# Kernel tuning notes

Hardware: AMD Instinct MI355X
Metric: run time of the kernel (lower is better)

The kernel has to match this reference:

```python
import jax, jax.numpy as jnp
import numpy as np

HEADS = 8
IN_CH = 768
INNER = 768
DK = INNER // HEADS


def setup_inputs() -> dict:
    key = jax.random.key(0)
    ks = jax.random.split(key, 9)
    bs, hw = 16, 1024
    s = 1.0 / np.sqrt(IN_CH)
    sp = 1.0 / np.sqrt(INNER)
    return {
        "x": jax.random.normal(ks[0], (bs, hw, IN_CH), jnp.float32),
        # weights stored (in, out) so y = x @ W + b (equiv to torch Linear)
        "Wq": jax.random.uniform(ks[1], (IN_CH, INNER), jnp.float32, -s, s),
        "bq": jax.random.uniform(ks[2], (INNER,), jnp.float32, -s, s),
        "Wk": jax.random.uniform(ks[3], (IN_CH, INNER), jnp.float32, -s, s),
        "bk": jax.random.uniform(ks[4], (INNER,), jnp.float32, -s, s),
        "Wv": jax.random.uniform(ks[5], (IN_CH, INNER), jnp.float32, -s, s),
        "bv": jax.random.uniform(ks[6], (INNER,), jnp.float32, -s, s),
        "Wp": jax.random.uniform(ks[7], (INNER, IN_CH), jnp.float32, -sp, sp),
        "bp": jax.random.uniform(ks[8], (IN_CH,), jnp.float32, -sp, sp),
    }


def reference(x, Wq, bq, Wk, bk, Wv, bv, Wp, bp):
    bs, hw, _ = x.shape
    # NOTE: the original torch code does .view(bs, heads, hw, dk) on a
    # (bs, hw, inner) tensor — a raw row-major reshape, not a head-split
    # transpose. Replicate exactly.
    q = (x @ Wq + bq).reshape(bs, HEADS, hw, DK)
    k = (x @ Wk + bk).reshape(bs, HEADS, hw, DK)
    v = (x @ Wv + bv).reshape(bs, HEADS, hw, DK)
    logits = jnp.einsum("bhqd,bhkd->bhqk", q, k) / np.sqrt(DK).astype(np.float32)
    attn = jax.nn.softmax(logits, axis=-1)
    out = jnp.einsum("bhqk,bhkd->bhqd", attn, v).reshape(bs, hw, INNER)
    # dropout is identity in eval mode
    return out @ Wp + bp
```

## Files before the change

### kernel.cpp

```cpp
#include <hip/hip_runtime.h>
#include <math.h>

typedef __bf16 bf16;
typedef __attribute__((ext_vector_type(8))) __bf16 bf16x8;
typedef __attribute__((ext_vector_type(4))) __bf16 bf16x4;
typedef __attribute__((ext_vector_type(4))) float f32x4;
typedef __attribute__((ext_vector_type(16))) float f32x16;

#define CE 0.14724445f

__global__ __launch_bounds__(256) void cvt_x(const float* __restrict__ x, bf16* __restrict__ xb) {
    size_t i = ((size_t)blockIdx.x * 256 + threadIdx.x) * 4;
    f32x4 v = *(const f32x4*)(x + i);
    bf16x4 o;
    o[0] = (bf16)v[0]; o[1] = (bf16)v[1]; o[2] = (bf16)v[2]; o[3] = (bf16)v[3];
    *(bf16x4*)(xb + i) = o;
}

struct WArgs { const float* w[4]; };

__global__ __launch_bounds__(256) void transpose_w(WArgs wa, bf16* __restrict__ out) {
    __shared__ float t[32][33];
    const int z = blockIdx.z;
    const float* __restrict__ W = wa.w[z];
    bf16* __restrict__ Wt = out + (size_t)z * 589824;
    int k0 = blockIdx.x * 32, n0 = blockIdx.y * 32;
    int tx = threadIdx.x, ty = threadIdx.y;
#pragma unroll
    for (int j = 0; j < 4; ++j)
        t[ty + j * 8][tx] = W[(size_t)(k0 + ty + j * 8) * 768 + n0 + tx];
    __syncthreads();
#pragma unroll
    for (int j = 0; j < 4; ++j)
        Wt[(size_t)(n0 + ty + j * 8) * 768 + k0 + tx] = (bf16)t[tx][ty + j * 8];
}

struct GemmArgs {
    const bf16* Bt[3];
    const float* bias[3];
    void* out[3];
};

template <bool F32OUT>
__global__ __launch_bounds__(256, 2) void gemm_kernel(const bf16* __restrict__ A, GemmArgs ga) {
    __shared__ __align__(16) bf16 As[128 * 64];
    __shared__ __align__(16) bf16 Bs[128 * 64];
    const int z = blockIdx.z;
    const bf16* __restrict__ Bt = ga.Bt[z];
    const int m0 = blockIdx.x * 128;
    const int n0 = blockIdx.y * 128;
    const int tid = threadIdx.x;
    const int lane = tid & 63, l15 = lane & 15, lq = lane >> 4;
    const int wid = tid >> 6;
    const int wm = (wid >> 1) * 64, wn = (wid & 1) * 64;

    f32x4 acc[4][4] = {};

    const int srow = tid >> 1;
    const int sc0 = (tid & 1) * 4;
    const bf16* __restrict__ Arow = A + (size_t)(m0 + srow) * 768;
    const bf16* __restrict__ Brow = Bt + (size_t)(n0 + srow) * 768;
    const int swz = srow & 7;

    for (int ks = 0; ks < 768; ks += 64) {
#pragma unroll
        for (int i = 0; i < 4; ++i) {
            int c = sc0 + i;
            bf16x8 av = *(const bf16x8*)(Arow + ks + c * 8);
            bf16x8 bv = *(const bf16x8*)(Brow + ks + c * 8);
            int sc = c ^ swz;
            *(bf16x8*)(As + srow * 64 + sc * 8) = av;
            *(bf16x8*)(Bs + srow * 64 + sc * 8) = bv;
        }
        __syncthreads();
#pragma unroll
        for (int kk = 0; kk < 2; ++kk) {
            bf16x8 af[4], bfr[4];
#pragma unroll
            for (int f = 0; f < 4; ++f) {
                int ar = wm + f * 16 + l15;
                int ac = (kk * 4 + lq) ^ (ar & 7);
                af[f] = *(const bf16x8*)(As + ar * 64 + ac * 8);
                int br = wn + f * 16 + l15;
                int bc = (kk * 4 + lq) ^ (br & 7);
                bfr[f] = *(const bf16x8*)(Bs + br * 64 + bc * 8);
            }
#pragma unroll
            for (int mf = 0; mf < 4; ++mf)
#pragma unroll
                for (int nf = 0; nf < 4; ++nf)
                    acc[mf][nf] = __builtin_amdgcn_mfma_f32_16x16x32_bf16(af[mf], bfr[nf], acc[mf][nf], 0, 0, 0);
        }
        __syncthreads();
    }
    const float* __restrict__ bias = ga.bias[z];
#pragma unroll
    for (int nf = 0; nf < 4; ++nf) {
        int col = n0 + wn + nf * 16 + l15;
        float bv = bias[col];
#pragma unroll
        for (int mf = 0; mf < 4; ++mf) {
            int rbase = m0 + wm + mf * 16 + lq * 4;
#pragma unroll
            for (int i = 0; i < 4; ++i) {
                float v = acc[mf][nf][i] + bv;
                if constexpr (F32OUT)
                    ((float*)ga.out[z])[(size_t)(rbase + i) * 768 + col] = v;
                else
                    ((bf16*)ga.out[z])[(size_t)(rbase + i) * 768 + col] = (bf16)v;
            }
        }
    }
}

__global__ __launch_bounds__(256) void transpose_v(const bf16* __restrict__ V, bf16* __restrict__ Vt) {
    __shared__ unsigned short t[64 * 97];
    const int g = blockIdx.y;
    const int kv0 = blockIdx.x * 64;
    const unsigned short* __restrict__ Vg = (const unsigned short*)V + (size_t)g * 98304;
    unsigned short* __restrict__ Vtg = (unsigned short*)Vt + (size_t)g * 98304;
    const int tid = threadIdx.x;
#pragma unroll
    for (int p = 0; p < 24; ++p) {
        int id = tid + p * 256;
        int row = id / 96, col = id % 96;
        t[row * 97 + col] = Vg[(size_t)(kv0 + row) * 96 + col];
    }
    __syncthreads();
#pragma unroll
    for (int p = 0; p < 24; ++p) {
        int id = tid + p * 256;
        int d = id >> 6, j = id & 63;
        Vtg[(size_t)d * 1024 + kv0 + j] = t[j * 97 + d];
    }
}

static __device__ inline int pk2(float a, float b) {
    union { __bf16 h[2]; int w; } u;
    u.h[0] = (__bf16)a; u.h[1] = (__bf16)b;
    return u.w;
}

static __device__ inline bf16x8 pack_step(float p0, float p1, float p2, float p3,
                                          float p4, float p5, float p6, float p7, int hi) {
    int A0 = pk2(p0, p1), A1 = pk2(p2, p3);
    int B0 = pk2(p4, p5), B1 = pk2(p6, p7);
    int t0 = hi ? A0 : B0;
    int t1 = hi ? A1 : B1;
    int x0 = __shfl_xor(t0, 32);
    int x1 = __shfl_xor(t1, 32);
    union { int w[4]; bf16x8 v; } u;
    u.w[0] = hi ? x0 : A0;
    u.w[1] = hi ? x1 : A1;
    u.w[2] = hi ? B0 : x0;
    u.w[3] = hi ? B1 : x1;
    return u.v;
}

__global__ __launch_bounds__(256, 3) void attn_kernel(const bf16* __restrict__ Q, const bf16* __restrict__ K,
                                                      const bf16* __restrict__ Vt, bf16* __restrict__ AO) {
    __shared__ __align__(16) bf16 Ks[64 * 128];
    __shared__ __align__(16) bf16 Vs[96 * 64];
    const int g = blockIdx.x;
    const int q0 = blockIdx.y * 128;
    const int tid = threadIdx.x;
    const int lane = tid & 63;
    const int l31 = lane & 31;
    const int hi = lane >> 5;
    const int wid = tid >> 6;
    const int qrow = q0 + wid * 32 + l31;
    const int sw = l31 & 7;
    const size_t gbase = (size_t)g * 98304;
    const bf16* __restrict__ Qg = Q + gbase;
    const bf16* __restrict__ Kg = K + gbase;
    const bf16* __restrict__ Vg = Vt + gbase;
    bf16* __restrict__ Og = AO + gbase;

    int koff[3], kld[3], voff[3], vld[3];
#pragma unroll
    for (int i = 0; i < 3; ++i) {
        int id = tid + i * 256;
        int kr = id / 12, kc = id - kr * 12;
        koff[i] = kr * 96 + kc * 8;
        kld[i] = kr * 128 + (kc ^ (kr & 7)) * 8;
        int vr = id >> 3, vc = id & 7;
        voff[i] = vr * 1024 + vc * 8;
        vld[i] = vr * 64 + (vc ^ (vr & 7)) * 8;
    }

    bf16x8 qf[6];
#pragma unroll
    for (int kk = 0; kk < 6; ++kk)
        qf[kk] = *(const bf16x8*)(Qg + (size_t)qrow * 96 + kk * 16 + hi * 8);

    f32x16 o[3] = {};
    float mrun = -INFINITY, lrun = 0.f;

    bf16x8 kst[3], vst[3];
#pragma unroll
    for (int i = 0; i < 3; ++i) {
        kst[i] = *(const bf16x8*)(Kg + koff[i]);
        vst[i] = *(const bf16x8*)(Vg + voff[i]);
    }

    for (int kt = 0; kt < 16; ++kt) {
        __syncthreads();
#pragma unroll
        for (int i = 0; i < 3; ++i) {
            *(bf16x8*)(Ks + kld[i]) = kst[i];
            *(bf16x8*)(Vs + vld[i]) = vst[i];
        }
        __syncthreads();
        if (kt < 15) {
            const int kvn = (kt + 1) * 64;
#pragma unroll
            for (int i = 0; i < 3; ++i) {
                kst[i] = *(const bf16x8*)(Kg + (size_t)kvn * 96 + koff[i]);
                vst[i] = *(const bf16x8*)(Vg + kvn + voff[i]);
            }
        }

        f32x16 s0 = {}, s1 = {};
#pragma unroll
        for (int kk = 0; kk < 6; ++kk) {
            int slot = ((kk * 2 + hi) ^ sw) * 8;
            bf16x8 k0 = *(const bf16x8*)(Ks + l31 * 128 + slot);
            bf16x8 k1 = *(const bf16x8*)(Ks + (l31 + 32) * 128 + slot);
            s0 = __builtin_amdgcn_mfma_f32_32x32x16_bf16(k0, qf[kk], s0, 0, 0, 0);
            s1 = __builtin_amdgcn_mfma_f32_32x32x16_bf16(k1, qf[kk], s1, 0, 0, 0);
        }
        float mx = s0[0];
#pragma unroll
        for (int r = 1; r < 16; ++r) mx = fmaxf(mx, s0[r]);
#pragma unroll
        for (int r = 0; r < 16; ++r) mx = fmaxf(mx, s1[r]);
        mx = fmaxf(mx, __shfl_xor(mx, 32));
        float newm = fmaxf(mrun, mx);
        float alpha = __builtin_amdgcn_exp2f(CE * (mrun - newm));
        mrun = newm;
        float lsum = 0.f;
#pragma unroll
        for (int r = 0; r < 16; ++r) {
            float p = __builtin_amdgcn_exp2f(CE * (s0[r] - newm));
            s0[r] = p; lsum += p;
        }
#pragma unroll
        for (int r = 0; r < 16; ++r) {
            float p = __builtin_amdgcn_exp2f(CE * (s1[r] - newm));
            s1[r] = p; lsum += p;
        }
        lsum += __shfl_xor(lsum, 32);
        lrun = lrun * alpha + lsum;
#pragma unroll
        for (int df = 0; df < 3; ++df)
#pragma unroll
            for (int r = 0; r < 16; ++r) o[df][r] *= alpha;

        bf16x8 pb0 = pack_step(s0[0], s0[1], s0[2], s0[3], s0[4], s0[5], s0[6], s0[7], hi);
        bf16x8 pb1 = pack_step(s0[8], s0[9], s0[10], s0[11], s0[12], s0[13], s0[14], s0[15], hi);
        bf16x8 pb2 = pack_step(s1[0], s1[1], s1[2], s1[3], s1[4], s1[5], s1[6], s1[7], hi);
        bf16x8 pb3 = pack_step(s1[8], s1[9], s1[10], s1[11], s1[12], s1[13], s1[14], s1[15], hi);
#pragma unroll
        for (int df = 0; df < 3; ++df) {
            const bf16* vrow = Vs + (df * 32 + l31) * 64;
            bf16x8 v0 = *(const bf16x8*)(vrow + ((0 + hi) ^ sw) * 8);
            bf16x8 v1 = *(const bf16x8*)(vrow + ((2 + hi) ^ sw) * 8);
            bf16x8 v2 = *(const bf16x8*)(vrow + ((4 + hi) ^ sw) * 8);
            bf16x8 v3 = *(const bf16x8*)(vrow + ((6 + hi) ^ sw) * 8);
            o[df] = __builtin_amdgcn_mfma_f32_32x32x16_bf16(v0, pb0, o[df], 0, 0, 0);
            o[df] = __builtin_amdgcn_mfma_f32_32x32x16_bf16(v1, pb1, o[df], 0, 0, 0);
            o[df] = __builtin_amdgcn_mfma_f32_32x32x16_bf16(v2, pb2, o[df], 0, 0, 0);
            o[df] = __builtin_amdgcn_mfma_f32_32x32x16_bf16(v3, pb3, o[df], 0, 0, 0);
        }
    }

    float inv = 1.0f / lrun;
#pragma unroll
    for (int df = 0; df < 3; ++df)
#pragma unroll
        for (int rq = 0; rq < 4; ++rq) {
            bf16x4 ov;
#pragma unroll
            for (int j = 0; j < 4; ++j) ov[j] = (bf16)(o[df][rq * 4 + j] * inv);
            *(bf16x4*)(Og + (size_t)qrow * 96 + df * 32 + rq * 8 + hi * 4) = ov;
        }
}

extern "C" void kernel_launch(void* const* d_in, const int* in_sizes, int n_in,
                              void* d_out, int out_size, void* d_ws, size_t ws_size,
                              hipStream_t stream) {
    const float* x  = (const float*)d_in[0];
    const float* Wq = (const float*)d_in[1];
    const float* bq = (const float*)d_in[2];
    const float* Wk = (const float*)d_in[3];
    const float* bk = (const float*)d_in[4];
    const float* Wv = (const float*)d_in[5];
    const float* bv = (const float*)d_in[6];
    const float* Wp = (const float*)d_in[7];
    const float* bp = (const float*)d_in[8];

    char* ws = (char*)d_ws;
    bf16* xb  = (bf16*)(ws);
    bf16* wt  = (bf16*)(ws + 25165824);
    bf16* Qb  = (bf16*)(ws + 29884416);
    bf16* Kb  = (bf16*)(ws + 55050240);
    bf16* Vb  = (bf16*)(ws + 80216064);
    bf16* Vtb = (bf16*)(ws + 105381888);
    bf16* AO  = xb;

    cvt_x<<<12288, 256, 0, stream>>>(x, xb);

    WArgs wa;
    wa.w[0] = Wq; wa.w[1] = Wk; wa.w[2] = Wv; wa.w[3] = Wp;
    transpose_w<<<dim3(24, 24, 4), dim3(32, 8), 0, stream>>>(wa, wt);

    GemmArgs g1{};
    g1.Bt[0] = wt;            g1.Bt[1] = wt + 589824;  g1.Bt[2] = wt + 2 * 589824;
    g1.bias[0] = bq;          g1.bias[1] = bk;         g1.bias[2] = bv;
    g1.out[0] = Qb;           g1.out[1] = Kb;          g1.out[2] = Vb;
    gemm_kernel<false><<<dim3(128, 6, 3), 256, 0, stream>>>(xb, g1);

    transpose_v<<<dim3(16, 128), 256, 0, stream>>>(Vb, Vtb);

    attn_kernel<<<dim3(128, 8), 256, 0, stream>>>(Qb, Kb, Vtb, AO);

    GemmArgs g2{};
    g2.Bt[0] = wt + 3 * 589824; g2.bias[0] = bp; g2.out[0] = (void*)d_out;
    g2.Bt[1] = g2.Bt[0]; g2.Bt[2] = g2.Bt[0];
    g2.bias[1] = bp; g2.bias[2] = bp;
    g2.out[1] = g2.out[0]; g2.out[2] = g2.out[0];
    gemm_kernel<true><<<dim3(128, 6, 1), 256, 0, stream>>>(AO, g2);
}
```

Before: 229.0 us.

## Use direct global-to-LDS loads, XCD-aware GEMM block remap, lazy softmax rescale

The GEMM and attention kernels now fill shared memory with global_load_lds DMA instead of register staging. GEMM blocks are launched on a 1D grid and remapped so neighbouring tiles land on the same XCD. In attention, V gets double buffering and K is prefetched right after the QK MFMAs, with s_setprio around the MFMA sections. The online softmax skips the max update and accumulator rescale unless the new row max exceeds the running max by a threshold. Together these aim to cut VGPR pressure, load latency and per-tile rescale work, at the cost of more LDS and a less exact running max that could overflow if the threshold is poorly chosen.

```diff
diff --git a/kernel.cpp b/kernel.cpp
--- a/kernel.cpp
+++ b/kernel.cpp
@@ -8,6 +8,12 @@
 typedef __attribute__((ext_vector_type(16))) float f32x16;
 
 #define CE 0.14724445f
+#define THR_RAW 54.0f
+
+#define GLOAD16(g, l)                                                          \
+    __builtin_amdgcn_global_load_lds(                                          \
+        (const __attribute__((address_space(1))) void*)(g),                    \
+        (__attribute__((address_space(3))) void*)(l), 16, 0, 0)
 
 __global__ __launch_bounds__(256) void cvt_x(const float* __restrict__ x, bf16* __restrict__ xb) {
     size_t i = ((size_t)blockIdx.x * 256 + threadIdx.x) * 4;
@@ -45,32 +51,38 @@
 __global__ __launch_bounds__(256, 2) void gemm_kernel(const bf16* __restrict__ A, GemmArgs ga) {
     __shared__ __align__(16) bf16 As[128 * 64];
     __shared__ __align__(16) bf16 Bs[128 * 64];
-    const int z = blockIdx.z;
+    const int nwg = gridDim.x;
+    const int bid = blockIdx.x;
+    const int lid = (bid & 7) * (nwg >> 3) + (bid >> 3);
+    const int z = lid / 768;
+    const int rem = lid - z * 768;
+    const int m0 = (rem / 6) * 128;
+    const int n0 = (rem % 6) * 128;
     const bf16* __restrict__ Bt = ga.Bt[z];
-    const int m0 = blockIdx.x * 128;
-    const int n0 = blockIdx.y * 128;
     const int tid = threadIdx.x;
     const int lane = tid & 63, l15 = lane & 15, lq = lane >> 4;
     const int wid = tid >> 6;
     const int wm = (wid >> 1) * 64, wn = (wid & 1) * 64;
 
+    const bf16* asrc[4]; const bf16* bsrc[4]; bf16* adst[4]; bf16* bdst[4];
+#pragma unroll
+    for (int i = 0; i < 4; ++i) {
+        int r = (wid * 4 + i) * 8 + (lane >> 3);
+        int s = lane & 7;
+        int c = s ^ (r & 7);
+        asrc[i] = A + (size_t)(m0 + r) * 768 + c * 8;
+        bsrc[i] = Bt + (size_t)(n0 + r) * 768 + c * 8;
+        adst[i] = As + (wid * 4 + i) * 512;
+        bdst[i] = Bs + (wid * 4 + i) * 512;
+    }
+
     f32x4 acc[4][4] = {};
 
-    const int srow = tid >> 1;
-    const int sc0 = (tid & 1) * 4;
-    const bf16* __restrict__ Arow = A + (size_t)(m0 + srow) * 768;
-    const bf16* __restrict__ Brow = Bt + (size_t)(n0 + srow) * 768;
-    const int swz = srow & 7;
-
     for (int ks = 0; ks < 768; ks += 64) {
 #pragma unroll
         for (int i = 0; i < 4; ++i) {
-            int c = sc0 + i;
-            bf16x8 av = *(const bf16x8*)(Arow + ks + c * 8);
-            bf16x8 bv = *(const bf16x8*)(Brow + ks + c * 8);
-            int sc = c ^ swz;
-            *(bf16x8*)(As + srow * 64 + sc * 8) = av;
-            *(bf16x8*)(Bs + srow * 64 + sc * 8) = bv;
+            GLOAD16(asrc[i] + ks, adst[i]);
+            GLOAD16(bsrc[i] + ks, bdst[i]);
         }
         __syncthreads();
 #pragma unroll
@@ -160,32 +172,37 @@
 __global__ __launch_bounds__(256, 3) void attn_kernel(const bf16* __restrict__ Q, const bf16* __restrict__ K,
                                                       const bf16* __restrict__ Vt, bf16* __restrict__ AO) {
     __shared__ __align__(16) bf16 Ks[64 * 128];
-    __shared__ __align__(16) bf16 Vs[96 * 64];
+    __shared__ __align__(16) bf16 Vss[2 * 96 * 64];
     const int g = blockIdx.x;
     const int q0 = blockIdx.y * 128;
     const int tid = threadIdx.x;
     const int lane = tid & 63;
-    const int l31 = lane & 31;
-    const int hi = lane >> 5;
-    const int wid = tid >> 6;
+    const int l31 = lane & 31, hi = lane >> 5, wid = tid >> 6;
+    const int sw = l31 & 7;
     const int qrow = q0 + wid * 32 + l31;
-    const int sw = l31 & 7;
     const size_t gbase = (size_t)g * 98304;
     const bf16* __restrict__ Qg = Q + gbase;
     const bf16* __restrict__ Kg = K + gbase;
     const bf16* __restrict__ Vg = Vt + gbase;
     bf16* __restrict__ Og = AO + gbase;
 
-    int koff[3], kld[3], voff[3], vld[3];
+    const bf16* ksrc[4]; bf16* kdst[4];
+#pragma unroll
+    for (int i = 0; i < 4; ++i) {
+        int r = (wid * 4 + i) * 4 + (lane >> 4);
+        int s = lane & 15;
+        int c = s ^ (r & 7);
+        ksrc[i] = Kg + r * 96 + c * 8;
+        kdst[i] = Ks + (wid * 4 + i) * 512;
+    }
+    const bf16* vsrc[3]; int vdoff[3];
 #pragma unroll
     for (int i = 0; i < 3; ++i) {
-        int id = tid + i * 256;
-        int kr = id / 12, kc = id - kr * 12;
-        koff[i] = kr * 96 + kc * 8;
-        kld[i] = kr * 128 + (kc ^ (kr & 7)) * 8;
-        int vr = id >> 3, vc = id & 7;
-        voff[i] = vr * 1024 + vc * 8;
-        vld[i] = vr * 64 + (vc ^ (vr & 7)) * 8;
+        int r = (wid * 3 + i) * 8 + (lane >> 3);
+        int s = lane & 7;
+        int c = s ^ (r & 7);
+        vsrc[i] = Vg + (size_t)r * 1024 + c * 8;
+        vdoff[i] = (wid * 3 + i) * 512;
     }
 
     bf16x8 qf[6];
@@ -193,34 +210,22 @@
     for (int kk = 0; kk < 6; ++kk)
         qf[kk] = *(const bf16x8*)(Qg + (size_t)qrow * 96 + kk * 16 + hi * 8);
 
+#pragma unroll
+    for (int i = 0; i < 4; ++i) GLOAD16(ksrc[i], kdst[i]);
+#pragma unroll
+    for (int i = 0; i < 3; ++i) GLOAD16(vsrc[i], Vss + vdoff[i]);
+    __syncthreads();
+#pragma unroll
+    for (int i = 0; i < 3; ++i) GLOAD16(vsrc[i] + 64, Vss + 6144 + vdoff[i]);
+
     f32x16 o[3] = {};
     float mrun = -INFINITY, lrun = 0.f;
 
-    bf16x8 kst[3], vst[3];
-#pragma unroll
-    for (int i = 0; i < 3; ++i) {
-        kst[i] = *(const bf16x8*)(Kg + koff[i]);
-        vst[i] = *(const bf16x8*)(Vg + voff[i]);
-    }
-
     for (int kt = 0; kt < 16; ++kt) {
-        __syncthreads();
-#pragma unroll
-        for (int i = 0; i < 3; ++i) {
-            *(bf16x8*)(Ks + kld[i]) = kst[i];
-            *(bf16x8*)(Vs + vld[i]) = vst[i];
-        }
-        __syncthreads();
-        if (kt < 15) {
-            const int kvn = (kt + 1) * 64;
-#pragma unroll
-            for (int i = 0; i < 3; ++i) {
-                kst[i] = *(const bf16x8*)(Kg + (size_t)kvn * 96 + koff[i]);
-                vst[i] = *(const bf16x8*)(Vg + kvn + voff[i]);
-            }
-        }
+        const bf16* Vcur = Vss + (kt & 1) * 6144;
 
         f32x16 s0 = {}, s1 = {};
+        __builtin_amdgcn_s_setprio(1);
 #pragma unroll
         for (int kk = 0; kk < 6; ++kk) {
             int slot = ((kk * 2 + hi) ^ sw) * 8;
@@ -229,40 +234,57 @@
             s0 = __builtin_amdgcn_mfma_f32_32x32x16_bf16(k0, qf[kk], s0, 0, 0, 0);
             s1 = __builtin_amdgcn_mfma_f32_32x32x16_bf16(k1, qf[kk], s1, 0, 0, 0);
         }
-        float mx = s0[0];
-#pragma unroll
-        for (int r = 1; r < 16; ++r) mx = fmaxf(mx, s0[r]);
-#pragma unroll
-        for (int r = 0; r < 16; ++r) mx = fmaxf(mx, s1[r]);
-        mx = fmaxf(mx, __shfl_xor(mx, 32));
-        float newm = fmaxf(mrun, mx);
-        float alpha = __builtin_amdgcn_exp2f(CE * (mrun - newm));
-        mrun = newm;
-        float lsum = 0.f;
+        __builtin_amdgcn_s_setprio(0);
+        __syncthreads();
+        if (kt < 15) {
+#pragma unroll
+            for (int i = 0; i < 4; ++i) GLOAD16(ksrc[i] + (kt + 1) * 6144, kdst[i]);
+        }
+
+        float t0 = fmaxf(fmaxf(s0[0], s0[1]), fmaxf(s0[2], s0[3]));
+        float t1 = fmaxf(fmaxf(s0[4], s0[5]), fmaxf(s0[6], s0[7]));
+        float t2 = fmaxf(fmaxf(s0[8], s0[9]), fmaxf(s0[10], s0[11]));
+        float t3 = fmaxf(fmaxf(s0[12], s0[13]), fmaxf(s0[14], s0[15]));
+        float u0 = fmaxf(fmaxf(s1[0], s1[1]), fmaxf(s1[2], s1[3]));
+        float u1 = fmaxf(fmaxf(s1[4], s1[5]), fmaxf(s1[6], s1[7]));
+        float u2 = fmaxf(fmaxf(s1[8], s1[9]), fmaxf(s1[10], s1[11]));
+        float u3 = fmaxf(fmaxf(s1[12], s1[13]), fmaxf(s1[14], s1[15]));
+        float pmax = fmaxf(fmaxf(fmaxf(t0, t1), fmaxf(t2, t3)),
+                           fmaxf(fmaxf(u0, u1), fmaxf(u2, u3)));
+        pmax = fmaxf(pmax, __shfl_xor(pmax, 32));
+        if (!__all(pmax - mrun <= THR_RAW)) {
+            float newm = fmaxf(mrun, pmax);
+            float alpha = __builtin_amdgcn_exp2f(CE * (mrun - newm));
+            mrun = newm;
+            lrun *= alpha;
+#pragma unroll
+            for (int df = 0; df < 3; ++df)
+#pragma unroll
+                for (int r = 0; r < 16; ++r) o[df][r] *= alpha;
+        }
+        float lsa = 0.f, lsb = 0.f;
 #pragma unroll
         for (int r = 0; r < 16; ++r) {
-            float p = __builtin_amdgcn_exp2f(CE * (s0[r] - newm));
-            s0[r] = p; lsum += p;
+            float p = __builtin_amdgcn_exp2f(CE * (s0[r] - mrun));
+            s0[r] = p; lsa += p;
         }
 #pragma unroll
         for (int r = 0; r < 16; ++r) {
-            float p = __builtin_amdgcn_exp2f(CE * (s1[r] - newm));
-            s1[r] = p; lsum += p;
-        }
+            float p = __builtin_amdgcn_exp2f(CE * (s1[r] - mrun));
+            s1[r] = p; lsb += p;
+        }
+        float lsum = lsa + lsb;
         lsum += __shfl_xor(lsum, 32);
-        lrun = lrun * alpha + lsum;
-#pragma unroll
-        for (int df = 0; df < 3; ++df)
-#pragma unroll
-            for (int r = 0; r < 16; ++r) o[df][r] *= alpha;
+        lrun += lsum;
 
         bf16x8 pb0 = pack_step(s0[0], s0[1], s0[2], s0[3], s0[4], s0[5], s0[6], s0[7], hi);
         bf16x8 pb1 = pack_step(s0[8], s0[9], s0[10], s0[11], s0[12], s0[13], s0[14], s0[15], hi);
         bf16x8 pb2 = pack_step(s1[0], s1[1], s1[2], s1[3], s1[4], s1[5], s1[6], s1[7], hi);
         bf16x8 pb3 = pack_step(s1[8], s1[9], s1[10], s1[11], s1[12], s1[13], s1[14], s1[15], hi);
+        __builtin_amdgcn_s_setprio(1);
 #pragma unroll
         for (int df = 0; df < 3; ++df) {
-            const bf16* vrow = Vs + (df * 32 + l31) * 64;
+            const bf16* vrow = Vcur + (df * 32 + l31) * 64;
             bf16x8 v0 = *(const bf16x8*)(vrow + ((0 + hi) ^ sw) * 8);
             bf16x8 v1 = *(const bf16x8*)(vrow + ((2 + hi) ^ sw) * 8);
             bf16x8 v2 = *(const bf16x8*)(vrow + ((4 + hi) ^ sw) * 8);
@@ -271,6 +293,13 @@
             o[df] = __builtin_amdgcn_mfma_f32_32x32x16_bf16(v1, pb1, o[df], 0, 0, 0);
             o[df] = __builtin_amdgcn_mfma_f32_32x32x16_bf16(v2, pb2, o[df], 0, 0, 0);
             o[df] = __builtin_amdgcn_mfma_f32_32x32x16_bf16(v3, pb3, o[df], 0, 0, 0);
+        }
+        __builtin_amdgcn_s_setprio(0);
+        __syncthreads();
+        if (kt < 14) {
+#pragma unroll
+            for (int i = 0; i < 3; ++i)
+                GLOAD16(vsrc[i] + (kt + 2) * 64, Vss + (kt & 1) * 6144 + vdoff[i]);
         }
     }
 
@@ -318,7 +347,7 @@
     g1.Bt[0] = wt;            g1.Bt[1] = wt + 589824;  g1.Bt[2] = wt + 2 * 589824;
     g1.bias[0] = bq;          g1.bias[1] = bk;         g1.bias[2] = bv;
     g1.out[0] = Qb;           g1.out[1] = Kb;          g1.out[2] = Vb;
-    gemm_kernel<false><<<dim3(128, 6, 3), 256, 0, stream>>>(xb, g1);
+    gemm_kernel<false><<<2304, 256, 0, stream>>>(xb, g1);
 
     transpose_v<<<dim3(16, 128), 256, 0, stream>>>(Vb, Vtb);
 
@@ -329,5 +358,5 @@
     g2.Bt[1] = g2.Bt[0]; g2.Bt[2] = g2.Bt[0];
     g2.bias[1] = bp; g2.bias[2] = bp;
     g2.out[1] = g2.out[0]; g2.out[2] = g2.out[0];
-    gemm_kernel<true><<<dim3(128, 6, 1), 256, 0, stream>>>(AO, g2);
-}
+    gemm_kernel<true><<<768, 256, 0, stream>>>(AO, g2);
+}
```

Measured after the change: 197.2 us. 1.16x faster.
